# Optimization experiments

Measured on AMD Instinct MI355X. Metric: run time of the kernel, lower is better.

## Reference

```python
import jax, jax.numpy as jnp
import numpy as np

B, L, D, H = 16, 1024, 1024, 16
HD = D // H  # head dim = 64


def setup_inputs() -> dict:
    rng = jax.random.key(0)
    ks = jax.random.split(rng, 12)
    s = 0.02
    return {
        "key": jax.random.normal(ks[0], (B, L, D), jnp.float32),
        "value": jax.random.normal(ks[1], (B, L, D), jnp.float32),
        "query": jax.random.normal(ks[2], (B, L, D), jnp.float32),
        "atten_masks": jax.random.randint(ks[3], (B, L, L), 0, 2, jnp.int32),
        "Wk": jax.random.normal(ks[4], (D, D), jnp.float32) * s,
        "bk": jnp.zeros((D,), jnp.float32),
        "Wq": jax.random.normal(ks[5], (D, D), jnp.float32) * s,
        "bq": jnp.zeros((D,), jnp.float32),
        "Wv": jax.random.normal(ks[6], (D, D), jnp.float32) * s,
        "bv": jnp.zeros((D,), jnp.float32),
        "Wp": jax.random.normal(ks[7], (D, D), jnp.float32) * s,
        "bp": jnp.zeros((D,), jnp.float32),
    }


def reference(key, value, query, atten_masks, Wk, bk, Wq, bq, Wv, bv, Wp, bp):
    # Linear projections (torch nn.Linear: x @ W^T + b)
    def lin(x, W, b):
        return x @ W.T + b

    # [B, L, D] -> [B, H, L, HD]
    def heads(x):
        return x.reshape(B, L, H, HD).transpose(0, 2, 1, 3)

    k = heads(lin(key, Wk, bk))
    q = heads(lin(query, Wq, bq))
    v = heads(lin(value, Wv, bv))

    scale = 1.0 / np.sqrt(HD).astype(np.float32)
    att = jnp.einsum("bhqd,bhkd->bhqk", q, k) * scale  # [B, H, L, L]
    att = jnp.where(atten_masks[:, None, :, :] == 0, -jnp.inf, att)
    att = jax.nn.softmax(att, axis=-1)

    y = jnp.einsum("bhqk,bhkd->bhqd", att, v)  # [B, H, L, HD]
    y = y.transpose(0, 2, 1, 3).reshape(B, L, D)
    return lin(y, Wp, bp)
```

## Files before the change

### kernel.cpp

```cpp
#include <hip/hip_runtime.h>

typedef __bf16 bf16_t;
typedef __bf16 bf16x4 __attribute__((ext_vector_type(4)));
typedef __bf16 bf16x8 __attribute__((ext_vector_type(8)));
typedef float f32x4 __attribute__((ext_vector_type(4)));
typedef float f32x16 __attribute__((ext_vector_type(16)));
typedef unsigned u32x2 __attribute__((ext_vector_type(2)));

#define QSCALE 0.18033688f

__device__ __forceinline__ int swz(int row) { return (row ^ (row >> 3)) & 7; }
__device__ __forceinline__ int swz2(int row) { return (row ^ (row >> 2)) & 3; }

__device__ __forceinline__ f32x4 mfma16(bf16x8 a, bf16x8 b, f32x4 c) {
  return __builtin_amdgcn_mfma_f32_16x16x32_bf16(a, b, c, 0, 0, 0);
}
__device__ __forceinline__ f32x16 mfma32(bf16x8 a, bf16x8 b, f32x16 c) {
  return __builtin_amdgcn_mfma_f32_32x32x16_bf16(a, b, c, 0, 0, 0);
}

__device__ __forceinline__ void gl_lds16(const void* g, void* l) {
  __builtin_amdgcn_global_load_lds(
      (const __attribute__((address_space(1))) unsigned int*)g,
      (__attribute__((address_space(3))) unsigned int*)l, 16, 0, 0);
}

__global__ __launch_bounds__(256) void cvt_all_kernel(
    const float* __restrict__ key, const float* __restrict__ query,
    const float* __restrict__ value, const float* __restrict__ Wk,
    const float* __restrict__ Wq, const float* __restrict__ Wv,
    const float* __restrict__ Wp, const int* __restrict__ mask,
    bf16_t* __restrict__ I1, bf16_t* __restrict__ I2, bf16_t* __restrict__ I3,
    bf16_t* __restrict__ Wkb, bf16_t* __restrict__ Wqb,
    bf16_t* __restrict__ Wvb, bf16_t* __restrict__ Wpb,
    unsigned* __restrict__ mbits) {
  const int bid = blockIdx.x;
  if (bid >= 53248) {
    int idx = (bid - 53248) * 256 + threadIdx.x;
    const int4* src = (const int4*)(mask + (size_t)idx * 32);
    unsigned w = 0;
#pragma unroll
    for (int i = 0; i < 8; ++i) {
      int4 v = src[i];
      w |= (v.x != 0 ? 1u : 0u) << (i * 4 + 0);
      w |= (v.y != 0 ? 1u : 0u) << (i * 4 + 1);
      w |= (v.z != 0 ? 1u : 0u) << (i * 4 + 2);
      w |= (v.w != 0 ? 1u : 0u) << (i * 4 + 3);
    }
    mbits[idx] = w;
    return;
  }
  const float* s;
  bf16_t* d;
  int base;
  float sc = 1.0f;
  if (bid < 16384) { s = key; d = I1; base = bid; }
  else if (bid < 32768) { s = query; d = I2; base = bid - 16384; }
  else if (bid < 49152) { s = value; d = I3; base = bid - 32768; }
  else if (bid < 50176) { s = Wk; d = Wkb; base = bid - 49152; }
  else if (bid < 51200) { s = Wq; d = Wqb; base = bid - 50176; sc = QSCALE; }
  else if (bid < 52224) { s = Wv; d = Wvb; base = bid - 51200; }
  else { s = Wp; d = Wpb; base = bid - 52224; }
  int i = base * 256 + threadIdx.x;
  float4 v = ((const float4*)s)[i];
  bf16x4 o;
  o[0] = (bf16_t)(v.x * sc); o[1] = (bf16_t)(v.y * sc);
  o[2] = (bf16_t)(v.z * sc); o[3] = (bf16_t)(v.w * sc);
  ((bf16x4*)d)[i] = o;
}

template <typename OT>
__device__ __forceinline__ void gemm256_body(const bf16_t* __restrict__ A,
                                             const bf16_t* __restrict__ W,
                                             const float* __restrict__ bias,
                                             float bscale,
                                             OT* __restrict__ O) {
  extern __shared__ __align__(16) char smem[];
  bf16_t* AsBase = (bf16_t*)smem;
  bf16_t* BsBase = (bf16_t*)(smem + 3 * 8192 * 2);

  const int t = threadIdx.x;
  const int lane = t & 63;
  const int wid = t >> 6;
  const int g = lane >> 4;
  const int lr = lane & 15;
  const int wm = wid >> 2, wn = wid & 3;
  const int lid = blockIdx.x;
  const int logical = (lid & 7) * 32 + (lid >> 3);
  const int m0 = (logical >> 2) * 256;
  const int n0 = (logical & 3) * 256;

  f32x4 acc[8][4] = {};

  auto STAGE = [&](int buf, int kb) {
    bf16_t* Ab = AsBase + buf * 8192;
    bf16_t* Bb = BsBase + buf * 8192;
#pragma unroll
    for (int rr = 0; rr < 2; ++rr) {
      int s = rr * 512 + t;
      int row = s >> 2, c = s & 3;
      gl_lds16(A + (size_t)(m0 + row) * 1024 + kb + (c ^ swz2(row)) * 8,
               &Ab[(rr * 512 + wid * 64) * 8]);
      gl_lds16(W + (size_t)(n0 + row) * 1024 + kb + (c ^ swz2(row)) * 8,
               &Bb[(rr * 512 + wid * 64) * 8]);
    }
  };

  STAGE(0, 0);
  STAGE(1, 32);

  int cur = 0;
  for (int kb = 0; kb < 1024; kb += 32) {
    if (kb + 32 < 1024)
      asm volatile("s_waitcnt vmcnt(4)" ::: "memory");
    else
      asm volatile("s_waitcnt vmcnt(0)" ::: "memory");
    __builtin_amdgcn_sched_barrier(0);
    __builtin_amdgcn_s_barrier();
    __builtin_amdgcn_sched_barrier(0);

    if (kb + 64 < 1024) {
      int fut = cur + 2;
      if (fut >= 3) fut -= 3;
      STAGE(fut, kb + 64);
    }

    const bf16_t* Ab = AsBase + cur * 8192;
    const bf16_t* Bb = BsBase + cur * 8192;
    bf16x8 a[8], b[4];
#pragma unroll
    for (int i = 0; i < 8; ++i) {
      int row = wm * 128 + i * 16 + lr;
      a[i] = *(const bf16x8*)&Ab[row * 32 + ((g ^ swz2(row))) * 8];
    }
#pragma unroll
    for (int j = 0; j < 4; ++j) {
      int row = wn * 64 + j * 16 + lr;
      b[j] = *(const bf16x8*)&Bb[row * 32 + ((g ^ swz2(row))) * 8];
    }
    __builtin_amdgcn_s_setprio(1);
#pragma unroll
    for (int i = 0; i < 8; ++i)
#pragma unroll
      for (int j = 0; j < 4; ++j)
        acc[i][j] = mfma16(a[i], b[j], acc[i][j]);
    __builtin_amdgcn_s_setprio(0);

    cur = (cur == 2) ? 0 : cur + 1;
  }

  float bval[4];
#pragma unroll
  for (int j = 0; j < 4; ++j)
    bval[j] = bias[n0 + wn * 64 + j * 16 + lr] * bscale;
#pragma unroll
  for (int i = 0; i < 8; ++i)
#pragma unroll
    for (int r = 0; r < 4; ++r) {
      int row = m0 + wm * 128 + i * 16 + g * 4 + r;
#pragma unroll
      for (int j = 0; j < 4; ++j) {
        int n = n0 + wn * 64 + j * 16 + lr;
        O[(size_t)row * 1024 + n] = (OT)(acc[i][j][r] + bval[j]);
      }
    }
}

__global__ __launch_bounds__(512, 2) void gemm256_qkv_kernel(
    const bf16_t* key, const bf16_t* query, const bf16_t* value,
    const bf16_t* Wkb, const bf16_t* Wqb, const bf16_t* Wvb, const float* bk,
    const float* bq, const float* bv, bf16_t* ko, bf16_t* qo, bf16_t* vo) {
  const bf16_t *A, *W;
  const float* bi;
  bf16_t* O;
  float bs = 1.0f;
  if (blockIdx.y == 0) { A = key; W = Wkb; bi = bk; O = ko; }
  else if (blockIdx.y == 1) { A = query; W = Wqb; bi = bq; O = qo; bs = QSCALE; }
  else { A = value; W = Wvb; bi = bv; O = vo; }
  gemm256_body<bf16_t>(A, W, bi, bs, O);
}

__global__ __launch_bounds__(512, 2) void gemm256_out_kernel(
    const bf16_t* __restrict__ A, const bf16_t* __restrict__ W,
    const float* __restrict__ b, float* __restrict__ O) {
  gemm256_body<float>(A, W, b, 1.0f, O);
}

__global__ __launch_bounds__(256) void transpose_v_kernel(
    const bf16_t* __restrict__ v_ws, bf16_t* __restrict__ vT) {
  __shared__ bf16_t T[64 * 66];
  const int kc = blockIdx.x, h = blockIdx.y, b = blockIdx.z;
  const int t = threadIdx.x;
  {
    int key = t >> 2, dblk = t & 3;
    const bf16_t* src =
        v_ws + ((size_t)(b * 1024 + kc * 64 + key)) * 1024 + h * 64 + dblk * 16;
    bf16x8 a0 = *(const bf16x8*)src;
    bf16x8 a1 = *(const bf16x8*)(src + 8);
    bf16_t* row = &T[key * 66 + dblk * 16];
#pragma unroll
    for (int j = 0; j < 4; ++j) {
      ((unsigned*)row)[j] = ((const unsigned*)&a0)[j];
      ((unsigned*)row)[j + 4] = ((const unsigned*)&a1)[j];
    }
  }
  __syncthreads();
  {
    int d = t >> 2, kcl = t & 3;
    bf16x8 o0, o1;
#pragma unroll
    for (int e = 0; e < 8; ++e) {
      o0[e] = T[(kcl * 16 + e) * 66 + d];
      o1[e] = T[(kcl * 16 + 8 + e) * 66 + d];
    }
    bf16_t* dst =
        vT + ((size_t)((b * 16 + h) * 64 + d)) * 1024 + kc * 64 + kcl * 16;
    *(bf16x8*)dst = o0;
    *(bf16x8*)(dst + 8) = o1;
  }
}

__global__ __launch_bounds__(256) void attn_kernel(
    const bf16_t* __restrict__ q_ws, const bf16_t* __restrict__ k_ws,
    const bf16_t* __restrict__ vT, const unsigned* __restrict__ mbits,
    bf16_t* __restrict__ y_ws) {
  __shared__ __align__(16) bf16_t Ks[128 * 64];
  __shared__ __align__(16) bf16_t Vs[64 * 128];

  const int lid = blockIdx.x;
  const int logical = (lid & 7) * 256 + (lid >> 3);
  const int qb = logical & 7;
  const int h = (logical >> 3) & 15;
  const int b = logical >> 7;
  const int t = threadIdx.x, lane = t & 63, wid = t >> 6;
  const int ql = lane & 31;
  const int hh = lane >> 5;
  const int q = qb * 128 + wid * 32 + ql;

  bf16x8 qf[4];
  {
    const bf16_t* qp = q_ws + ((size_t)(b * 1024 + q)) * 1024 + h * 64 + hh * 8;
#pragma unroll
    for (int kc = 0; kc < 4; ++kc) qf[kc] = *(const bf16x8*)(qp + kc * 16);
  }

  bf16x8 onesf;
#pragma unroll
  for (int e = 0; e < 8; ++e) onesf[e] = (bf16_t)1.0f;

  f32x16 acc0 = {}, acc1 = {}, accl = {};
  const bf16_t* Kb = k_ws + ((size_t)b * 1024) * 1024 + h * 64;
  const bf16_t* Vb = vT + ((size_t)((b * 16 + h) * 64)) * 1024;
  const unsigned* mrow = mbits + ((size_t)(b * 1024 + q)) * 32;

  for (int kb = 0; kb < 8; ++kb) {
    __syncthreads();
#pragma unroll
    for (int rr = 0; rr < 4; ++rr) {
      int s = rr * 256 + t;
      int row = s >> 3, c = s & 7;
      gl_lds16(Kb + (size_t)(kb * 128 + row) * 1024 + (c ^ swz(row)) * 8,
               &Ks[(rr * 256 + wid * 64) * 8]);
    }
#pragma unroll
    for (int rr = 0; rr < 4; ++rr) {
      int s = rr * 256 + t;
      int row = s >> 4, c = s & 15;
      gl_lds16(Vb + (size_t)row * 1024 + kb * 128 + ((c ^ swz(row))) * 8,
               &Vs[(rr * 256 + wid * 64) * 8]);
    }
    uint4 mw = *(const uint4*)&mrow[kb * 4];
    __syncthreads();

#pragma unroll
    for (int ct = 0; ct < 4; ++ct) {
      f32x16 c = {};
      __builtin_amdgcn_s_setprio(1);
#pragma unroll
      for (int kc = 0; kc < 4; ++kc) {
        int row = ct * 32 + ql;
        bf16x8 kf = *(const bf16x8*)&Ks[row * 64 + (((kc * 2 + hh) ^ swz(row))) * 8];
        c = mfma32(kf, qf[kc], c);
      }
      __builtin_amdgcn_s_setprio(0);

      unsigned w = ((const unsigned*)&mw)[ct] >> (4 * hh);
      float p[16];
#pragma unroll
      for (int r = 0; r < 16; ++r) {
        const int posr = (r & 3) + 8 * (r >> 2);
        int nm = (int)(w << (31 - posr)) >> 31;
        float e0 = __builtin_amdgcn_exp2f(c[r]);
        p[r] = __int_as_float(__float_as_int(e0) & nm);
      }

      bf16x8 pbt[2];
#pragma unroll
      for (int j = 0; j < 2; ++j) {
        const int base = j * 8;
        union { bf16_t h[2]; unsigned u; } a0, a1, b0, b1;
        a0.h[0] = (bf16_t)p[base + 0]; a0.h[1] = (bf16_t)p[base + 1];
        a1.h[0] = (bf16_t)p[base + 2]; a1.h[1] = (bf16_t)p[base + 3];
        b0.h[0] = (bf16_t)p[base + 4]; b0.h[1] = (bf16_t)p[base + 5];
        b1.h[0] = (bf16_t)p[base + 6]; b1.h[1] = (bf16_t)p[base + 7];
        u32x2 s0 = __builtin_amdgcn_permlane32_swap(a0.u, b0.u, false, false);
        u32x2 s1 = __builtin_amdgcn_permlane32_swap(a1.u, b1.u, false, false);
        union { unsigned u[4]; bf16x8 v; } pk;
        pk.u[0] = s0.x;
        pk.u[1] = s1.x;
        pk.u[2] = s0.y;
        pk.u[3] = s1.y;
        pbt[j] = pk.v;
      }

      __builtin_amdgcn_s_setprio(1);
#pragma unroll
      for (int j = 0; j < 2; ++j) {
        int sl = (2 * ct + j) * 2 + hh;
        {
          int row = ql;
          bf16x8 vf = *(const bf16x8*)&Vs[row * 128 + ((sl ^ swz(row))) * 8];
          acc0 = mfma32(vf, pbt[j], acc0);
        }
        {
          int row = 32 + ql;
          bf16x8 vf = *(const bf16x8*)&Vs[row * 128 + ((sl ^ swz(row))) * 8];
          acc1 = mfma32(vf, pbt[j], acc1);
        }
        accl = mfma32(onesf, pbt[j], accl);
      }
      __builtin_amdgcn_s_setprio(0);
    }
  }

  float inv = 1.0f / fmaxf(accl[0], 1e-30f);
  bf16_t* yp = y_ws + ((size_t)(b * 1024 + q)) * 1024 + h * 64;
#pragma unroll
  for (int j = 0; j < 4; ++j) {
    bf16x4 o0, o1;
#pragma unroll
    for (int e = 0; e < 4; ++e) {
      o0[e] = (bf16_t)(acc0[4 * j + e] * inv);
      o1[e] = (bf16_t)(acc1[4 * j + e] * inv);
    }
    *(bf16x4*)&yp[8 * j + 4 * hh] = o0;
    *(bf16x4*)&yp[32 + 8 * j + 4 * hh] = o1;
  }
}

extern "C" void kernel_launch(void* const* d_in, const int* in_sizes, int n_in,
                              void* d_out, int out_size, void* d_ws,
                              size_t ws_size, hipStream_t stream) {
  (void)in_sizes; (void)n_in; (void)out_size; (void)ws_size;
  const float* key = (const float*)d_in[0];
  const float* value = (const float*)d_in[1];
  const float* query = (const float*)d_in[2];
  const int* mask = (const int*)d_in[3];
  const float* Wk = (const float*)d_in[4];
  const float* bk = (const float*)d_in[5];
  const float* Wq = (const float*)d_in[6];
  const float* bq = (const float*)d_in[7];
  const float* Wv = (const float*)d_in[8];
  const float* bv = (const float*)d_in[9];
  const float* Wp = (const float*)d_in[10];
  const float* bp = (const float*)d_in[11];
  float* out = (float*)d_out;

  char* ws = (char*)d_ws;
  const size_t MB = 1ull << 20;
  unsigned* mbits = (unsigned*)(ws);
  bf16_t* Wkb = (bf16_t*)(ws + 2 * MB);
  bf16_t* Wqb = (bf16_t*)(ws + 4 * MB);
  bf16_t* Wvb = (bf16_t*)(ws + 6 * MB);
  bf16_t* Wpb = (bf16_t*)(ws + 8 * MB);
  bf16_t* I1 = (bf16_t*)(ws + 10 * MB);
  bf16_t* I2 = (bf16_t*)(ws + 42 * MB);
  bf16_t* I3 = (bf16_t*)(ws + 74 * MB);
  bf16_t* k_ws = (bf16_t*)(ws + 106 * MB);
  bf16_t* q_ws = (bf16_t*)(ws + 138 * MB);
  bf16_t* v_ws = (bf16_t*)(ws + 170 * MB);
  bf16_t* vT_ws = I1;
  bf16_t* y_ws = I2;

  const size_t GEMM_LDS = 3 * 8192 * 2 * 2;

  cvt_all_kernel<<<55296, 256, 0, stream>>>(key, query, value, Wk, Wq, Wv, Wp,
                                            mask, I1, I2, I3, Wkb, Wqb, Wvb,
                                            Wpb, mbits);
  gemm256_qkv_kernel<<<dim3(256, 3), 512, GEMM_LDS, stream>>>(
      I1, I2, I3, Wkb, Wqb, Wvb, bk, bq, bv, k_ws, q_ws, v_ws);
  transpose_v_kernel<<<dim3(16, 16, 16), 256, 0, stream>>>(v_ws, vT_ws);
  attn_kernel<<<2048, 256, 0, stream>>>(q_ws, k_ws, vT_ws, mbits, y_ws);
  gemm256_out_kernel<<<256, 512, GEMM_LDS, stream>>>(y_ws, Wpb, bp, out);
}
```

Baseline: 341.2 us.

## Split GEMM k-step into two half phases and widen V tile swizzle

The projection GEMM main loop now issues half of the next stage's global-to-LDS loads before each of two MFMA half-blocks, with an extra barrier between them. The intent is to spread load issue across the compute and lower register pressure by loading A fragments in two groups of four. Separately, the attention kernel's V tile swizzle now XORs over 16 chunks instead of 8, to cut LDS bank conflicts on its 128-wide rows. The added barrier per k-step adds synchronization cost.

```diff
diff --git a/kernel.cpp b/kernel.cpp
--- a/kernel.cpp
+++ b/kernel.cpp
@@ -11,6 +11,7 @@
 
 __device__ __forceinline__ int swz(int row) { return (row ^ (row >> 3)) & 7; }
 __device__ __forceinline__ int swz2(int row) { return (row ^ (row >> 2)) & 3; }
+__device__ __forceinline__ int swzv(int row) { return (row ^ (row >> 3)) & 15; }
 
 __device__ __forceinline__ f32x4 mfma16(bf16x8 a, bf16x8 b, f32x4 c) {
   return __builtin_amdgcn_mfma_f32_16x16x32_bf16(a, b, c, 0, 0, 0);
@@ -92,22 +93,19 @@
 
   f32x4 acc[8][4] = {};
 
-  auto STAGE = [&](int buf, int kb) {
+  auto STAGE_HALF = [&](int buf, int kb, int rr) {
     bf16_t* Ab = AsBase + buf * 8192;
     bf16_t* Bb = BsBase + buf * 8192;
-#pragma unroll
-    for (int rr = 0; rr < 2; ++rr) {
-      int s = rr * 512 + t;
-      int row = s >> 2, c = s & 3;
-      gl_lds16(A + (size_t)(m0 + row) * 1024 + kb + (c ^ swz2(row)) * 8,
-               &Ab[(rr * 512 + wid * 64) * 8]);
-      gl_lds16(W + (size_t)(n0 + row) * 1024 + kb + (c ^ swz2(row)) * 8,
-               &Bb[(rr * 512 + wid * 64) * 8]);
-    }
+    int s = rr * 512 + t;
+    int row = s >> 2, c = s & 3;
+    gl_lds16(A + (size_t)(m0 + row) * 1024 + kb + (c ^ swz2(row)) * 8,
+             &Ab[(rr * 512 + wid * 64) * 8]);
+    gl_lds16(W + (size_t)(n0 + row) * 1024 + kb + (c ^ swz2(row)) * 8,
+             &Bb[(rr * 512 + wid * 64) * 8]);
   };
 
-  STAGE(0, 0);
-  STAGE(1, 32);
+  STAGE_HALF(0, 0, 0);  STAGE_HALF(0, 0, 1);
+  STAGE_HALF(1, 32, 0); STAGE_HALF(1, 32, 1);
 
   int cur = 0;
   for (int kb = 0; kb < 1024; kb += 32) {
@@ -119,34 +117,53 @@
     __builtin_amdgcn_s_barrier();
     __builtin_amdgcn_sched_barrier(0);
 
-    if (kb + 64 < 1024) {
-      int fut = cur + 2;
-      if (fut >= 3) fut -= 3;
-      STAGE(fut, kb + 64);
-    }
-
+    const bool more = kb + 64 < 1024;
+    int fut = cur + 2;
+    if (fut >= 3) fut -= 3;
     const bf16_t* Ab = AsBase + cur * 8192;
     const bf16_t* Bb = BsBase + cur * 8192;
-    bf16x8 a[8], b[4];
-#pragma unroll
-    for (int i = 0; i < 8; ++i) {
-      int row = wm * 128 + i * 16 + lr;
-      a[i] = *(const bf16x8*)&Ab[row * 32 + ((g ^ swz2(row))) * 8];
-    }
+
+    if (more) STAGE_HALF(fut, kb + 64, 0);
+    bf16x8 b[4], a0[4];
 #pragma unroll
     for (int j = 0; j < 4; ++j) {
       int row = wn * 64 + j * 16 + lr;
       b[j] = *(const bf16x8*)&Bb[row * 32 + ((g ^ swz2(row))) * 8];
     }
+#pragma unroll
+    for (int i = 0; i < 4; ++i) {
+      int row = wm * 128 + i * 16 + lr;
+      a0[i] = *(const bf16x8*)&Ab[row * 32 + ((g ^ swz2(row))) * 8];
+    }
     __builtin_amdgcn_s_setprio(1);
 #pragma unroll
-    for (int i = 0; i < 8; ++i)
+    for (int i = 0; i < 4; ++i)
 #pragma unroll
       for (int j = 0; j < 4; ++j)
-        acc[i][j] = mfma16(a[i], b[j], acc[i][j]);
+        acc[i][j] = mfma16(a0[i], b[j], acc[i][j]);
     __builtin_amdgcn_s_setprio(0);
 
-    cur = (cur == 2) ? 0 : cur + 1;
+    __builtin_amdgcn_sched_barrier(0);
+    __builtin_amdgcn_s_barrier();
+    __builtin_amdgcn_sched_barrier(0);
+
+    if (more) STAGE_HALF(fut, kb + 64, 1);
+    bf16x8 a1[4];
+#pragma unroll
+    for (int i = 0; i < 4; ++i) {
+      int row = wm * 128 + (4 + i) * 16 + lr;
+      a1[i] = *(const bf16x8*)&Ab[row * 32 + ((g ^ swz2(row))) * 8];
+    }
+    __builtin_amdgcn_s_setprio(1);
+#pragma unroll
+    for (int i = 0; i < 4; ++i)
+#pragma unroll
+      for (int j = 0; j < 4; ++j)
+        acc[4 + i][j] = mfma16(a1[i], b[j], acc[4 + i][j]);
+    __builtin_amdgcn_s_setprio(0);
+
+    cur = cur + 1;
+    if (cur >= 3) cur -= 3;
   }
 
   float bval[4];
@@ -266,7 +283,7 @@
     for (int rr = 0; rr < 4; ++rr) {
       int s = rr * 256 + t;
       int row = s >> 4, c = s & 15;
-      gl_lds16(Vb + (size_t)row * 1024 + kb * 128 + ((c ^ swz(row))) * 8,
+      gl_lds16(Vb + (size_t)row * 1024 + kb * 128 + ((c ^ swzv(row))) * 8,
                &Vs[(rr * 256 + wid * 64) * 8]);
     }
     uint4 mw = *(const uint4*)&mrow[kb * 4];
@@ -319,12 +336,12 @@
         int sl = (2 * ct + j) * 2 + hh;
         {
           int row = ql;
-          bf16x8 vf = *(const bf16x8*)&Vs[row * 128 + ((sl ^ swz(row))) * 8];
+          bf16x8 vf = *(const bf16x8*)&Vs[row * 128 + ((sl ^ swzv(row))) * 8];
           acc0 = mfma32(vf, pbt[j], acc0);
         }
         {
           int row = 32 + ql;
-          bf16x8 vf = *(const bf16x8*)&Vs[row * 128 + ((sl ^ swz(row))) * 8];
+          bf16x8 vf = *(const bf16x8*)&Vs[row * 128 + ((sl ^ swzv(row))) * 8];
           acc1 = mfma32(vf, pbt[j], acc1);
         }
         accl = mfma32(onesf, pbt[j], accl);
```

Result: no change. 345.0 us (+1.1%).
